# Kernel optimization log

Hardware: AMD Instinct MI355X
Metric: run time of the kernel (lower is better)

## Reference

```python
import jax, jax.numpy as jnp
import numpy as np

TEMP = 10.0
D_IN, D_HID, D_OUT = 256, 512, 256
B, M = 4, 4096


def _mlp(x, W1, b1, W2, b2):
    # two-layer MLP, ReLU hidden, linear output ('cnt' = continuous)
    h = jax.nn.relu(jnp.einsum('bmd,dh->bmh', x, W1) + b1)
    return jnp.einsum('bmh,ho->bmo', h, W2) + b2


def setup_inputs() -> dict:
    key = jax.random.key(0)
    ks = jax.random.split(key, 9)
    s1 = 1.0 / np.sqrt(D_IN)
    s2 = 1.0 / np.sqrt(D_HID)
    return {
        'x': jax.random.normal(ks[0], (B, M, D_IN), dtype=jnp.float32),
        'Wq1': jax.random.normal(ks[1], (D_IN, D_HID), dtype=jnp.float32) * s1,
        'bq1': jnp.zeros((D_HID,), dtype=jnp.float32),
        'Wq2': jax.random.normal(ks[2], (D_HID, D_OUT), dtype=jnp.float32) * s2,
        'bq2': jnp.zeros((D_OUT,), dtype=jnp.float32),
        'Wk1': jax.random.normal(ks[3], (D_IN, D_HID), dtype=jnp.float32) * s1,
        'bk1': jnp.zeros((D_HID,), dtype=jnp.float32),
        'Wk2': jax.random.normal(ks[4], (D_HID, D_OUT), dtype=jnp.float32) * s2,
        'bk2': jnp.zeros((D_OUT,), dtype=jnp.float32),
    }


def reference(x, Wq1, bq1, Wq2, bq2, Wk1, bk1, Wk2, bk2):
    queries = _mlp(x, Wq1, bq1, Wq2, bq2)   # [B, M, D_OUT]
    keys = _mlp(x, Wk1, bk1, Wk2, bk2)      # [B, M, D_OUT]
    qkt = jnp.einsum('bnd,bmd->bnm', queries, keys)  # [B, M, M]
    row_max = jnp.max(qkt, axis=-1, keepdims=True)   # row-max normalization (not sqrt(d))
    dist = jax.nn.softmax(TEMP * qkt / row_max, axis=-1)
    return dist
```

## Files before the change

kernel.cpp:

```cpp
#include <hip/hip_runtime.h>
#include <hip/hip_bf16.h>

typedef unsigned short u16;
typedef unsigned int u32;
typedef _Float16 f16;
typedef __attribute__((ext_vector_type(4))) float f32x4;
typedef __attribute__((ext_vector_type(8))) short s16x8;
typedef __attribute__((ext_vector_type(8))) _Float16 f16x8;

__device__ __forceinline__ u16 f2bf(float f) {
    union { float f; u32 u; } v; v.f = f;
    u32 r = v.u + 0x7FFFu + ((v.u >> 16) & 1u);
    return (u16)(r >> 16);
}
__device__ __forceinline__ float bf2f(u16 h) {
    union { u32 u; float f; } v; v.u = ((u32)h) << 16;
    return v.f;
}

__device__ __forceinline__ void gll16(const void* g, void* l) {
    __builtin_amdgcn_global_load_lds(
        (const __attribute__((address_space(1))) void*)g,
        (__attribute__((address_space(3))) void*)l, 16, 0, 0);
}


__global__ __launch_bounds__(256) void split_x_kernel(
    const float* __restrict__ x, u16* __restrict__ hi, u16* __restrict__ lo) {
    int i = blockIdx.x * 256 + threadIdx.x;
    float4 v = ((const float4*)x)[i];
    u16 h0 = f2bf(v.x), h1 = f2bf(v.y), h2 = f2bf(v.z), h3 = f2bf(v.w);
    ushort4 h, l;
    h.x = h0; h.y = h1; h.z = h2; h.w = h3;
    l.x = f2bf(v.x - bf2f(h0)); l.y = f2bf(v.y - bf2f(h1));
    l.z = f2bf(v.z - bf2f(h2)); l.w = f2bf(v.w - bf2f(h3));
    ((ushort4*)hi)[i] = h; ((ushort4*)lo)[i] = l;
}

__global__ __launch_bounds__(256) void split_wT_kernel(
    const float* __restrict__ Wq1, const float* __restrict__ Wk1,
    const float* __restrict__ Wq2, const float* __restrict__ Wk2,
    u16* __restrict__ w1hi, u16* __restrict__ w1lo,
    u16* __restrict__ w2hi, u16* __restrict__ w2lo) {
    int y = blockIdx.y;
    const float* src = (y == 0) ? Wq1 : (y == 1) ? Wk1 : (y == 2) ? Wq2 : Wk2;
    int R = (y < 2) ? 256 : 512;
    int C = (y < 2) ? 512 : 256;
    u16* dh = ((y < 2) ? w1hi : w2hi) + (y & 1) * 131072;
    u16* dl = ((y < 2) ? w1lo : w2lo) + (y & 1) * 131072;
    int i = blockIdx.x * 256 + threadIdx.x;
    int c = i / R, r = i - c * R;
    float v = src[(size_t)r * C + c];
    u16 h = f2bf(v);
    dh[i] = h; dl[i] = f2bf(v - bf2f(h));
}

__global__ void pack_bias(const float* __restrict__ bq1, const float* __restrict__ bk1,
                          const float* __restrict__ bq2, const float* __restrict__ bk2,
                          float* __restrict__ b1, float* __restrict__ b2) {
    int t = threadIdx.x;
    b1[t] = bq1[t]; b1[512 + t] = bk1[t];
    if (t < 256) { b2[t] = bq2[t]; b2[256 + t] = bk2[t]; }
}

#define BM 128
#define BN 128
#define BK 64

template<int SPLIT_OUT, int RELU, int SPLITB, int F16S>
__global__ __launch_bounds__(256, 2)
void gemm_bt(const u16* __restrict__ Ahi, const u16* __restrict__ Alo,
             const u16* __restrict__ Bhi, const u16* __restrict__ Blo,
             const float* __restrict__ bias, long biasBatch,
             void* __restrict__ Cout, u16* __restrict__ Chi, u16* __restrict__ Clo,
             int M, int N, int K,
             long aBatch, long bBatch, long cBatch) {
    __shared__ u16 lds[(3 + SPLITB) * BM * BK];
    const int tid = threadIdx.x;
    const int wave = tid >> 6, lane = tid & 63;
    const int bz = blockIdx.z;
    const long m0 = (long)blockIdx.y * BM, n0 = (long)blockIdx.x * BN;

    const u16* pAhi = Ahi + (size_t)bz * aBatch;
    const u16* pAlo = Alo + (size_t)bz * aBatch;
    const u16* pBhi = Bhi + (size_t)bz * bBatch;
    const u16* pBlo = Blo + (size_t)bz * bBatch;

    int srow[4], scol[4];
#pragma unroll
    for (int i = 0; i < 4; i++) {
        int lin = wave * 4096 + i * 1024 + lane * 16;
        srow[i] = lin >> 7;
        scol[i] = (lin & 127) >> 1;
    }

    const int wr = wave >> 1, wc = wave & 1;
    const int lrow = lane & 15, kgrp = lane >> 4;

    f32x4 acc[4][4] = {};

    const int ksteps = K / BK;
    for (int kt = 0; kt < ksteps; ++kt) {
#pragma unroll
        for (int i = 0; i < 4; i++) {
            size_t ga = (size_t)(m0 + srow[i]) * K + (size_t)kt * BK + scol[i];
            size_t gb = (size_t)(n0 + srow[i]) * K + (size_t)kt * BK + scol[i];
            u32 lb = (u32)(wave * 4096 + i * 1024);
            gll16(pAhi + ga, (char*)lds + 0 * 16384 + lb);
            gll16(pAlo + ga, (char*)lds + 1 * 16384 + lb);
            gll16(pBhi + gb, (char*)lds + 2 * 16384 + lb);
            if constexpr (SPLITB) gll16(pBlo + gb, (char*)lds + 3 * 16384 + lb);
        }
        __syncthreads();
#pragma unroll
        for (int kk = 0; kk < 2; ++kk) {
            s16x8 ah[4], al[4], bh[4], bl[4];
            const int ko = kk * 32 + kgrp * 8;
#pragma unroll
            for (int m = 0; m < 4; m++) {
                int r = wr * 64 + m * 16 + lrow;
                ah[m] = *(const s16x8*)&lds[0 * 8192 + r * 64 + ko];
                al[m] = *(const s16x8*)&lds[1 * 8192 + r * 64 + ko];
            }
#pragma unroll
            for (int n = 0; n < 4; n++) {
                int r = wc * 64 + n * 16 + lrow;
                bh[n] = *(const s16x8*)&lds[2 * 8192 + r * 64 + ko];
                if constexpr (SPLITB) bl[n] = *(const s16x8*)&lds[3 * 8192 + r * 64 + ko];
            }
#pragma unroll
            for (int m = 0; m < 4; m++)
#pragma unroll
                for (int n = 0; n < 4; n++) {
                    acc[m][n] = __builtin_amdgcn_mfma_f32_16x16x32_bf16(ah[m], bh[n], acc[m][n], 0, 0, 0);
                    if constexpr (SPLITB)
                        acc[m][n] = __builtin_amdgcn_mfma_f32_16x16x32_bf16(ah[m], bl[n], acc[m][n], 0, 0, 0);
                    acc[m][n] = __builtin_amdgcn_mfma_f32_16x16x32_bf16(al[m], bh[n], acc[m][n], 0, 0, 0);
                }
        }
        __syncthreads();
    }

#pragma unroll
    for (int m = 0; m < 4; m++) {
#pragma unroll
        for (int n = 0; n < 4; n++) {
            long col = n0 + wc * 64 + n * 16 + lrow;
            float bv = 0.f;
            if (SPLIT_OUT) bv = bias[bz * biasBatch + col];
#pragma unroll
            for (int j = 0; j < 4; j++) {
                long row = m0 + wr * 64 + m * 16 + kgrp * 4 + j;
                float v = acc[m][n][j];
                size_t o = (size_t)bz * cBatch + (size_t)row * N + col;
                if constexpr (SPLIT_OUT) {
                    v += bv;
                    if (RELU) v = fmaxf(v, 0.f);
                    u16 h = f2bf(v);
                    Chi[o] = h;
                    Clo[o] = f2bf(v - bf2f(h));
                } else if constexpr (F16S) {
                    ((f16*)Cout)[o] = (f16)v;
                } else {
                    ((float*)Cout)[o] = v;
                }
            }
        }
    }
}

__global__ __launch_bounds__(256) void softmax_rows(float* __restrict__ S) {
    const int tid = threadIdx.x;
    float* p = S + (size_t)blockIdx.x * 4096;
    float4 v[4];
    float lmax = -3.4e38f;
#pragma unroll
    for (int i = 0; i < 4; i++) {
        v[i] = ((float4*)p)[tid + 256 * i];
        lmax = fmaxf(lmax, fmaxf(fmaxf(v[i].x, v[i].y), fmaxf(v[i].z, v[i].w)));
    }
#pragma unroll
    for (int o = 32; o; o >>= 1) lmax = fmaxf(lmax, __shfl_xor(lmax, o));
    __shared__ float redm[4];
    __shared__ float reds[4];
    if ((tid & 63) == 0) redm[tid >> 6] = lmax;
    __syncthreads();
    const float m = fmaxf(fmaxf(redm[0], redm[1]), fmaxf(redm[2], redm[3]));
    const float c = 10.0f / m;
    float s = 0.f;
#pragma unroll
    for (int i = 0; i < 4; i++) {
        v[i].x = expf(c * v[i].x - 10.0f);
        v[i].y = expf(c * v[i].y - 10.0f);
        v[i].z = expf(c * v[i].z - 10.0f);
        v[i].w = expf(c * v[i].w - 10.0f);
        s += v[i].x + v[i].y + v[i].z + v[i].w;
    }
#pragma unroll
    for (int o = 32; o; o >>= 1) s += __shfl_xor(s, o);
    if ((tid & 63) == 0) reds[tid >> 6] = s;
    __syncthreads();
    const float inv = 1.0f / (reds[0] + reds[1] + reds[2] + reds[3]);
#pragma unroll
    for (int i = 0; i < 4; i++) {
        v[i].x *= inv; v[i].y *= inv; v[i].z *= inv; v[i].w *= inv;
        ((float4*)p)[tid + 256 * i] = v[i];
    }
}

__global__ __launch_bounds__(256) void softmax_f16(const f16* __restrict__ S,
                                                   float* __restrict__ O) {
    const int tid = threadIdx.x;
    const f16* p = S + (size_t)blockIdx.x * 4096;
    float* o = O + (size_t)blockIdx.x * 4096;
    f16x8 a0 = ((const f16x8*)p)[tid];
    f16x8 a1 = ((const f16x8*)p)[tid + 256];
    float v[16];
#pragma unroll
    for (int j = 0; j < 8; j++) { v[j] = (float)a0[j]; v[8 + j] = (float)a1[j]; }
    float lmax = -3.4e38f;
#pragma unroll
    for (int j = 0; j < 16; j++) lmax = fmaxf(lmax, v[j]);
#pragma unroll
    for (int off = 32; off; off >>= 1) lmax = fmaxf(lmax, __shfl_xor(lmax, off));
    __shared__ float redm[4];
    __shared__ float reds[4];
    if ((tid & 63) == 0) redm[tid >> 6] = lmax;
    __syncthreads();
    const float m = fmaxf(fmaxf(redm[0], redm[1]), fmaxf(redm[2], redm[3]));
    const float c = 10.0f / m;
    float s = 0.f;
#pragma unroll
    for (int j = 0; j < 16; j++) { v[j] = expf(c * v[j] - 10.0f); s += v[j]; }
#pragma unroll
    for (int off = 32; off; off >>= 1) s += __shfl_xor(s, off);
    if ((tid & 63) == 0) reds[tid >> 6] = s;
    __syncthreads();
    const float inv = 1.0f / (reds[0] + reds[1] + reds[2] + reds[3]);
    float4 w;
#pragma unroll
    for (int q = 0; q < 4; q++) {
        int base = q * 4;
        w.x = v[base + 0] * inv; w.y = v[base + 1] * inv;
        w.z = v[base + 2] * inv; w.w = v[base + 3] * inv;
        int idx = (q < 2) ? (2 * tid + q) : (2 * tid + 512 + (q - 2));
        ((float4*)o)[idx] = w;
    }
}

extern "C" void kernel_launch(void* const* d_in, const int* in_sizes, int n_in,
                              void* d_out, int out_size, void* d_ws, size_t ws_size,
                              hipStream_t stream) {
    const float* x   = (const float*)d_in[0];
    const float* Wq1 = (const float*)d_in[1];
    const float* bq1 = (const float*)d_in[2];
    const float* Wq2 = (const float*)d_in[3];
    const float* bq2 = (const float*)d_in[4];
    const float* Wk1 = (const float*)d_in[5];
    const float* bk1 = (const float*)d_in[6];
    const float* Wk2 = (const float*)d_in[7];
    const float* bk2 = (const float*)d_in[8];
    float* out = (float*)d_out;

    const size_t MB = 1048576;
    char* ws = (char*)d_ws;
    float* b1 = (float*)(ws);
    float* b2 = (float*)(ws + 4096);
    u16* w1hi = (u16*)(ws + 8 * 1024);
    u16* w1lo = (u16*)(ws + 8 * 1024 + 512 * 1024);
    u16* w2hi = (u16*)(ws + 8 * 1024 + 1024 * 1024);
    u16* w2lo = (u16*)(ws + 8 * 1024 + 1536 * 1024);
    u16* qhi  = (u16*)(ws + 4 * MB);
    u16* khi  = (u16*)(ws + 12 * MB);
    u16* qlo  = (u16*)(ws + 20 * MB);
    u16* klo  = (u16*)(ws + 28 * MB);
    f16* S16  = (f16*)(ws + 36 * MB);

    const bool f16s = (ws_size >= 164 * MB);

    char* ob = (char*)d_out;
    u16* xhi = (u16*)(ob + 0 * MB);
    u16* xlo = (u16*)(ob + 8 * MB);
    u16* Hhi = (u16*)(ob + 16 * MB);
    u16* Hlo = (u16*)(ob + 48 * MB);

    split_x_kernel<<<4096, 256, 0, stream>>>(x, xhi, xlo);
    split_wT_kernel<<<dim3(512, 4), 256, 0, stream>>>(Wq1, Wk1, Wq2, Wk2,
                                                      w1hi, w1lo, w2hi, w2lo);
    pack_bias<<<1, 512, 0, stream>>>(bq1, bk1, bq2, bk2, b1, b2);

    gemm_bt<1, 1, 1, 0><<<dim3(4, 128, 2), 256, 0, stream>>>(
        xhi, xlo, w1hi, w1lo, b1, 512,
        nullptr, Hhi, Hlo,
        16384, 512, 256,
        0L, 131072L, 8388608L);

    gemm_bt<1, 0, 1, 0><<<dim3(2, 128, 2), 256, 0, stream>>>(
        Hhi, Hlo, w2hi, w2lo, b2, 256,
        nullptr, qhi, qlo,
        16384, 256, 512,
        8388608L, 131072L, 4194304L);

    if (f16s) {
        gemm_bt<0, 0, 0, 1><<<dim3(32, 32, 4), 256, 0, stream>>>(
            qhi, qlo, khi, klo, nullptr, 0,
            (void*)S16, nullptr, nullptr,
            4096, 4096, 256,
            1048576L, 1048576L, 16777216L);
        softmax_f16<<<16384, 256, 0, stream>>>(S16, out);
    } else {
        gemm_bt<0, 0, 0, 0><<<dim3(32, 32, 4), 256, 0, stream>>>(
            qhi, qlo, khi, klo, nullptr, 0,
            (void*)out, nullptr, nullptr,
            4096, 4096, 256,
            1048576L, 1048576L, 16777216L);
        softmax_rows<<<16384, 256, 0, stream>>>(out);
    }
}
```

Before: 472.9 us.

## Stage GEMM epilogue through LDS for vectorized stores and remap workgroups across XCDs

The block index is remapped so consecutive workgroups land on the same XCD chunk, which is meant to improve L2 locality of shared operand tiles on the multi-XCD MI355X. For the bf16-split and f16 outputs, the epilogue now writes the accumulator tile into swizzled LDS and then emits 16-byte coalesced global stores instead of scattered 2-byte stores. The cost is an extra barrier and an LDS round trip, and the fp32 output path is left unchanged.

Result: no change. 468.7 us (-0.9%).

```diff
diff --git a/kernel.cpp b/kernel.cpp
--- a/kernel.cpp
+++ b/kernel.cpp
@@ -78,8 +78,20 @@
     __shared__ u16 lds[(3 + SPLITB) * BM * BK];
     const int tid = threadIdx.x;
     const int wave = tid >> 6, lane = tid & 63;
-    const int bz = blockIdx.z;
-    const long m0 = (long)blockIdx.y * BM, n0 = (long)blockIdx.x * BN;
+
+    u32 gx = gridDim.x, gy = gridDim.y, gz = gridDim.z;
+    u32 flat = (blockIdx.z * gy + blockIdx.y) * gx + blockIdx.x;
+    u32 nwg = gx * gy * gz;
+    u32 bx, by, bz;
+    if ((nwg & 7u) == 0u) {
+        u32 cpx = nwg >> 3;
+        u32 nf = (flat & 7u) * cpx + (flat >> 3);
+        bx = nf % gx; u32 t = nf / gx; by = t % gy; bz = t / gy;
+    } else {
+        bx = blockIdx.x; by = blockIdx.y; bz = blockIdx.z;
+    }
+
+    const long m0 = (long)by * BM, n0 = (long)bx * BN;
 
     const u16* pAhi = Ahi + (size_t)bz * aBatch;
     const u16* pAlo = Alo + (size_t)bz * aBatch;
@@ -141,31 +153,63 @@
         __syncthreads();
     }
 
-#pragma unroll
-    for (int m = 0; m < 4; m++) {
-#pragma unroll
-        for (int n = 0; n < 4; n++) {
-            long col = n0 + wc * 64 + n * 16 + lrow;
-            float bv = 0.f;
-            if (SPLIT_OUT) bv = bias[bz * biasBatch + col];
-#pragma unroll
-            for (int j = 0; j < 4; j++) {
-                long row = m0 + wr * 64 + m * 16 + kgrp * 4 + j;
-                float v = acc[m][n][j];
-                size_t o = (size_t)bz * cBatch + (size_t)row * N + col;
-                if constexpr (SPLIT_OUT) {
-                    v += bv;
-                    if (RELU) v = fmaxf(v, 0.f);
-                    u16 h = f2bf(v);
-                    Chi[o] = h;
-                    Clo[o] = f2bf(v - bf2f(h));
-                } else if constexpr (F16S) {
-                    ((f16*)Cout)[o] = (f16)v;
-                } else {
-                    ((float*)Cout)[o] = v;
+    if constexpr (SPLIT_OUT || F16S) {
+        u16* sh  = (u16*)lds;
+        u16* slo = (u16*)lds + 16384;
+#pragma unroll
+        for (int m = 0; m < 4; m++) {
+#pragma unroll
+            for (int n = 0; n < 4; n++) {
+                int col_l = wc * 64 + n * 16 + lrow;
+                float bv = 0.f;
+                if constexpr (SPLIT_OUT) bv = bias[bz * biasBatch + n0 + col_l];
+#pragma unroll
+                for (int j = 0; j < 4; j++) {
+                    int row_l = wr * 64 + m * 16 + kgrp * 4 + j;
+                    int sc = col_l ^ (((row_l >> 2) & 3) << 4);
+                    float v = acc[m][n][j];
+                    if constexpr (SPLIT_OUT) {
+                        v += bv;
+                        if (RELU) v = fmaxf(v, 0.f);
+                        u16 h = f2bf(v);
+                        sh[row_l * 128 + sc]  = h;
+                        slo[row_l * 128 + sc] = f2bf(v - bf2f(h));
+                    } else {
+                        union { f16 f; u16 u; } cv; cv.f = (f16)v;
+                        sh[row_l * 128 + sc] = cv.u;
+                    }
                 }
             }
         }
+        __syncthreads();
+#pragma unroll
+        for (int i = 0; i < 8; i++) {
+            int idx = i * 256 + tid;
+            int row_l = idx >> 4;
+            int c8 = (idx & 15) << 3;
+            int sc = c8 ^ (((row_l >> 2) & 3) << 4);
+            size_t go = (size_t)bz * cBatch + (size_t)(m0 + row_l) * N + n0 + c8;
+            s16x8 vh = *(const s16x8*)&sh[row_l * 128 + sc];
+            if constexpr (SPLIT_OUT) {
+                s16x8 vl = *(const s16x8*)&slo[row_l * 128 + sc];
+                *(s16x8*)&Chi[go] = vh;
+                *(s16x8*)&Clo[go] = vl;
+            } else {
+                *(s16x8*)&((u16*)Cout)[go] = vh;
+            }
+        }
+    } else {
+#pragma unroll
+        for (int m = 0; m < 4; m++)
+#pragma unroll
+            for (int n = 0; n < 4; n++) {
+                long col = n0 + wc * 64 + n * 16 + lrow;
+#pragma unroll
+                for (int j = 0; j < 4; j++) {
+                    long row = m0 + wr * 64 + m * 16 + kgrp * 4 + j;
+                    ((float*)Cout)[(size_t)bz * cBatch + (size_t)row * N + col] = acc[m][n][j];
+                }
+            }
     }
 }
 
```
